# Optimization experiments

Hardware: AMD Instinct MI355X
Metric: run time of the kernel (lower is better)

Reference implementation:

```python
import jax, jax.numpy as jnp
import numpy as np

T, N, E, F, H, OUT = 6, 50000, 800000, 32, 64, 16


def _glorot(key, shape):
    lim = np.sqrt(6.0 / (shape[0] + shape[1])).astype(np.float32)
    return jax.random.uniform(key, shape, jnp.float32, -lim, lim)


def setup_inputs() -> dict:
    key = jax.random.key(0)
    ks = jax.random.split(key, 12)
    return {
        "xs": jax.random.normal(ks[0], (T, N, F), jnp.float32),
        "edge_index": jax.random.randint(ks[1], (T, 2, E), 0, N, jnp.int32),
        # GCNConv weights/biases for the z, r, h gates
        "Wz": _glorot(ks[2], (F, H)), "bz": jnp.zeros((H,), jnp.float32),
        "Wr": _glorot(ks[3], (F, H)), "br": jnp.zeros((H,), jnp.float32),
        "Wh": _glorot(ks[4], (F, H)), "bh": jnp.zeros((H,), jnp.float32),
        # Linear(2H -> H) per gate
        "Lz_W": _glorot(ks[5], (2 * H, H)), "Lz_b": jnp.zeros((H,), jnp.float32),
        "Lr_W": _glorot(ks[6], (2 * H, H)), "Lr_b": jnp.zeros((H,), jnp.float32),
        "Lh_W": _glorot(ks[7], (2 * H, H)), "Lh_b": jnp.zeros((H,), jnp.float32),
        # final Linear(H -> 16)
        "out_W": _glorot(ks[8], (H, OUT)), "out_b": jnp.zeros((OUT,), jnp.float32),
    }


def _gcn(x, W, b, src, dst):
    """GCNConv: D^-1/2 (A+I) D^-1/2 X W + b, edge list form."""
    n = x.shape[0]
    xw = x @ W  # [N,H] project first (cheaper than per-edge)
    loop = jnp.arange(n, dtype=src.dtype)
    s = jnp.concatenate([src, loop])
    d = jnp.concatenate([dst, loop])
    deg = jax.ops.segment_sum(jnp.ones_like(d, jnp.float32), d, num_segments=n)
    dinv = jnp.where(deg > 0, jax.lax.rsqrt(deg), 0.0)
    norm = dinv[s] * dinv[d]          # [E+N]
    msg = xw[s] * norm[:, None]       # gather + scale
    agg = jax.ops.segment_sum(msg, d, num_segments=n)  # scatter-add
    return agg + b


def reference(xs, edge_index, Wz, bz, Wr, br, Wh, bh,
              Lz_W, Lz_b, Lr_W, Lr_b, Lh_W, Lh_b, out_W, out_b):
    n = xs.shape[1]

    def step(h, inp):
        x, src, dst = inp
        Z = jax.nn.sigmoid(jnp.concatenate([_gcn(x, Wz, bz, src, dst), h], -1) @ Lz_W + Lz_b)
        R = jax.nn.sigmoid(jnp.concatenate([_gcn(x, Wr, br, src, dst), h], -1) @ Lr_W + Lr_b)
        Ht = jnp.tanh(jnp.concatenate([_gcn(x, Wh, bh, src, dst), h * R], -1) @ Lh_W + Lh_b)
        h_new = Z * h + (1.0 - Z) * Ht
        return h_new, None

    h0 = jnp.zeros((n, Wz.shape[1]), xs.dtype)
    h_final, _ = jax.lax.scan(step, h0, (xs, edge_index[:, 0], edge_index[:, 1]))
    return h_final @ out_W + out_b  # [N,16]
```

## Files before the change

kernel.cpp:

```cpp
#include <hip/hip_runtime.h>
#include <hip/hip_bf16.h>

#define TT 6
#define NN 50000
#define EE 800000
#define FF 32
#define HH 64
#define OO 16

#define NB 256
#define DPB 196
#define CHUNK 4096
#define CAP 4096

#define WFRAG_N 19456

typedef unsigned short ushort_t;
typedef unsigned char uchar_t;
typedef short short8 __attribute__((ext_vector_type(8)));
typedef float f32x4 __attribute__((ext_vector_type(4)));

__device__ __forceinline__ float ubf(ushort_t v){ return __uint_as_float(((unsigned)v) << 16); }
__device__ __forceinline__ ushort_t f2b(float f){
  unsigned u = __float_as_uint(f);
  return (ushort_t)((u + 0x7FFFu + ((u >> 16) & 1u)) >> 16);
}
__device__ __forceinline__ float lo16f(unsigned u){ return __uint_as_float(u << 16); }
__device__ __forceinline__ float hi16f(unsigned u){ return __uint_as_float(u & 0xFFFF0000u); }

__global__ void prepall_kernel(const float* __restrict__ Wz,const float* __restrict__ bz,
                               const float* __restrict__ Wr,const float* __restrict__ br,
                               const float* __restrict__ Wh,const float* __restrict__ bh,
                               const float* __restrict__ Lz,const float* __restrict__ Lzb,
                               const float* __restrict__ Lr,const float* __restrict__ Lrb,
                               const float* __restrict__ Lh,const float* __restrict__ Lhb,
                               const float* __restrict__ oW,const float* __restrict__ ob,
                               short* __restrict__ wfrag, float* __restrict__ wbias,
                               int* __restrict__ bcur){
  int bid = blockIdx.x, tid = threadIdx.x;
  if (bid < 76){
    int idx = bid*256 + tid;
    int slot = idx >> 9, lane = (idx >> 3) & 63, j = idx & 7;
    int q = lane >> 4, l15 = lane & 15;
    float val;
    if (slot < 36){
      int g, kc, ncol;
      if (slot < 24){ int nt = slot/3; kc = slot - nt*3; ncol = nt*16 + l15;
                      g = (ncol < 64) ? 0 : 1; ncol &= 63; }
      else          { int s2 = slot-24; int nt = s2/3; kc = s2 - nt*3;
                      ncol = nt*16 + l15; g = 2; }
      const float* W = (g==0)?Wz:((g==1)?Wr:Wh);
      const float* L = (g==0)?Lz:((g==1)?Lr:Lh);
      int k = kc*32 + q*8 + j;
      if (k < 32){
        float s = 0.f;
        for (int m = 0; m < 64; m++) s += W[k*64+m] * L[m*64+ncol];
        val = s;
      } else val = L[(32+k)*64 + ncol];
    } else {
      int kc = slot - 36;
      int k = kc*32 + q*8 + j;
      val = oW[k*16 + l15];
    }
    wfrag[idx] = (short)f2b(val);
  } else {
    if (tid < 192){
      int g = tid >> 6, j = tid & 63;
      const float* L  = (g==0)?Lz:((g==1)?Lr:Lh);
      const float* bb = (g==0)?bz:((g==1)?br:bh);
      const float* Lb = (g==0)?Lzb:((g==1)?Lrb:Lhb);
      float s = Lb[j];
      for (int m = 0; m < 64; m++) s += bb[m] * L[m*64+j];
      wbias[tid] = s;
    } else if (tid < 208){
      wbias[tid] = ob[tid-192];
    }
    for (int i = tid; i < 1536; i += 256) bcur[i] = 0;
  }
}

__global__ __launch_bounds__(256) void scatter_kernel(const int* __restrict__ ei,
                                                      int* __restrict__ bcur,
                                                      ushort_t* __restrict__ ssrc16,
                                                      uchar_t* __restrict__ sdst8){
  int t = blockIdx.y;
  __shared__ int cnt[NB];
  __shared__ int lstart[NB];
  __shared__ int gbase[NB];
  __shared__ int wsum[4];
  __shared__ ushort_t spay[CHUNK];
  __shared__ uchar_t  sdlo[CHUNK];
  __shared__ uchar_t  sbk[CHUNK];
  int tid = threadIdx.x;
  cnt[tid] = 0;
  __syncthreads();
  int e0 = blockIdx.x*CHUNK;
  const int* srcs = ei + t*2*EE;
  const int* dsts = ei + t*2*EE + EE;
  int pk[CHUNK/256];
  int ps[CHUNK/256];
  int pd[CHUNK/256];
  #pragma unroll
  for (int i = 0; i < CHUNK/256; i++){
    int e = e0 + i*256 + tid;
    if (e < EE){
      int s = srcs[e], d = dsts[e];
      int b = d / DPB;
      int lr = atomicAdd(&cnt[b], 1);
      pk[i] = (b << 12) | lr;
      ps[i] = s;
      pd[i] = d - b*DPB;
    } else pk[i] = -1;
  }
  __syncthreads();
  {
    int v = cnt[tid];
    int lane = tid & 63, wid = tid >> 6;
    int x = v;
    #pragma unroll
    for (int o = 1; o < 64; o <<= 1){
      int y = __shfl_up(x, o, 64);
      if (lane >= o) x += y;
    }
    if (lane == 63) wsum[wid] = x;
    __syncthreads();
    if (tid == 0){
      int s = 0;
      #pragma unroll
      for (int w = 0; w < 4; w++){ int tmp = wsum[w]; wsum[w] = s; s += tmp; }
    }
    __syncthreads();
    lstart[tid] = x - v + wsum[wid];
    gbase[tid] = (v > 0) ? atomicAdd(&bcur[t*NB + tid], v) : 0;
  }
  __syncthreads();
  #pragma unroll
  for (int i = 0; i < CHUNK/256; i++){
    if (pk[i] >= 0){
      int b = pk[i] >> 12, lr = pk[i] & 4095;
      int pos = lstart[b] + lr;
      spay[pos] = (ushort_t)ps[i];
      sdlo[pos] = (uchar_t)pd[i];
      sbk[pos]  = (uchar_t)b;
    }
  }
  __syncthreads();
  int nE = EE - e0; if (nE > CHUNK) nE = CHUNK;
  for (int i = tid; i < nE; i += 256){
    int b = sbk[i];
    int gpos = gbase[b] + (i - lstart[b]);
    if (gpos < CAP){
      size_t sb = (size_t)(t*NB + b)*CAP + gpos;
      ssrc16[sb] = spay[i];
      sdst8[sb]  = sdlo[i];
    }
  }
}

__global__ __launch_bounds__(256) void degdinv_kernel(const uchar_t* __restrict__ sdst8,
                                                      const int* __restrict__ bcur,
                                                      float* __restrict__ dinv){
  int b = blockIdx.x, t = blockIdx.y, tid = threadIdx.x;
  __shared__ int cnt[DPB];
  for (int i = tid; i < DPB; i += 256) cnt[i] = 0;
  __syncthreads();
  int ecnt = bcur[t*NB + b]; if (ecnt > CAP) ecnt = CAP;
  const uchar_t* dp = sdst8 + (size_t)(t*NB + b)*CAP;
  for (int i = tid; i < ecnt; i += 256)
    atomicAdd(&cnt[dp[i]], 1);
  __syncthreads();
  for (int i = tid; i < DPB; i += 256){
    int n = b*DPB + i;
    if (n < NN) dinv[t*NN + n] = rsqrtf((float)(cnt[i] + 1));
  }
}

__global__ void cvtscale_kernel(const float4* __restrict__ x4,
                                const float* __restrict__ dinv,
                                ushort4* __restrict__ xb4){
  int i = blockIdx.x*256 + threadIdx.x;
  if (i < TT*NN*8){
    float dn = dinv[i >> 3];
    float4 v = x4[i];
    ushort4 o;
    o.x = f2b(v.x*dn); o.y = f2b(v.y*dn); o.z = f2b(v.z*dn); o.w = f2b(v.w*dn);
    xb4[i] = o;
  }
}

__global__ __launch_bounds__(256) void gatherb_kernel(const ushort_t* __restrict__ xbs,
                                                      const ushort_t* __restrict__ ssrc16,
                                                      const uchar_t* __restrict__ sdst8,
                                                      const int* __restrict__ bcur,
                                                      ushort_t* __restrict__ aggb){
  int l = blockIdx.x;
  int wk = ((l & 7) * 192) + (l >> 3);
  int t = wk >> 8;
  int b = wk & 255;
  int tid = threadIdx.x;
  __shared__ ushort_t ssrc[CAP];
  __shared__ int scnt[DPB];
  __shared__ int soff[DPB + 1];
  __shared__ int scur[DPB];
  if (tid < DPB) scnt[tid] = 0;
  __syncthreads();
  int ecnt = bcur[t*NB + b]; if (ecnt > CAP) ecnt = CAP;
  size_t slab = (size_t)(t*NB + b)*CAP;
  const ushort_t* sp = ssrc16 + slab;
  const uchar_t*  dp = sdst8 + slab;
  for (int e = tid; e < ecnt; e += 256)
    atomicAdd(&scnt[dp[e]], 1);
  __syncthreads();
  if (tid < DPB) scur[tid] = scnt[tid];
  __syncthreads();
  for (int s = 1; s < DPB; s <<= 1){
    int v = 0;
    if (tid < DPB && tid >= s) v = scur[tid - s];
    __syncthreads();
    if (tid < DPB) scur[tid] += v;
    __syncthreads();
  }
  if (tid < DPB) soff[tid + 1] = scur[tid];
  if (tid == 0) soff[0] = 0;
  __syncthreads();
  if (tid < DPB) scur[tid] = soff[tid];
  __syncthreads();
  for (int e = tid; e < ecnt; e += 256){
    int ld = dp[e];
    int pos = atomicAdd(&scur[ld], 1);
    ssrc[pos] = sp[e];
  }
  __syncthreads();
  int wv = tid >> 6, lane = tid & 63;
  int g = lane >> 3, fp = lane & 7;
  const uint2* xb2 = (const uint2*)xbs + (size_t)t*NN*8;
  uint2* agg2 = (uint2*)aggb + (size_t)t*NN*8;
  for (int bb = wv; bb*8 < DPB; bb += 4){
    int ld = bb*8 + g;
    int e0 = 0, e1 = 0;
    if (ld < DPB){ e0 = soff[ld]; e1 = soff[ld + 1]; }
    float a0 = 0.f, a1 = 0.f, a2 = 0.f, a3 = 0.f;
    int i = e0;
    if (i < e1){
      int s = (int)ssrc[i];
      uint2 r = xb2[(size_t)s*8 + fp];
      for (++i; i < e1; ++i){
        int s2 = (int)ssrc[i];
        uint2 r2 = xb2[(size_t)s2*8 + fp];
        a0 += lo16f(r.x); a1 += hi16f(r.x);
        a2 += lo16f(r.y); a3 += hi16f(r.y);
        r = r2;
      }
      a0 += lo16f(r.x); a1 += hi16f(r.x);
      a2 += lo16f(r.y); a3 += hi16f(r.y);
    }
    int n = b*DPB + ld;
    if (ld < DPB && n < NN){
      float dn = rsqrtf((float)(e1 - e0 + 1));
      uint2 sv = xb2[(size_t)n*8 + fp];
      float o0 = dn*(a0 + lo16f(sv.x));
      float o1 = dn*(a1 + hi16f(sv.x));
      float o2 = dn*(a2 + lo16f(sv.y));
      float o3 = dn*(a3 + hi16f(sv.y));
      uint2 pk;
      pk.x = (unsigned)f2b(o0) | ((unsigned)f2b(o1) << 16);
      pk.y = (unsigned)f2b(o2) | ((unsigned)f2b(o3) << 16);
      agg2[(size_t)n*8 + fp] = pk;
    }
  }
}

__global__ __launch_bounds__(256) void gates_kernel(const ushort_t* __restrict__ aggb,
                                                    const float* __restrict__ wbias,
                                                    const short* __restrict__ wfrag,
                                                    float* __restrict__ out){
  __shared__ __align__(16) short As[2048];
  __shared__ __align__(16) short Hsp[4096];
  __shared__ __align__(16) short HRp[4096];
  int tid = threadIdx.x;
  int nb = blockIdx.x*64;
  int wv = tid >> 6, lane = tid & 63;
  int q = lane >> 4, l15 = lane & 15;
  #pragma unroll
  for (int r = 0; r < 8; r++) ((int*)Hsp)[tid + 256*r] = 0;
  short8 wz[3], wr[3], wh[3];
  #pragma unroll
  for (int kc = 0; kc < 3; kc++){
    wz[kc] = ((const short8*)wfrag)[(wv*3 + kc)*64 + lane];
    wr[kc] = ((const short8*)wfrag)[((wv+4)*3 + kc)*64 + lane];
    wh[kc] = ((const short8*)wfrag)[(24 + wv*3 + kc)*64 + lane];
  }
  int jz = wv*16 + l15;
  float cz = wbias[jz], cr = wbias[64 + jz], ch = wbias[128 + jz];
  int hidx = ((jz >> 3)*64)*8 + (jz & 7);
  f32x4 accZ[4], accR[4];
  for (int t = 0; t < TT; t++){
    {
      int n = tid >> 2, c = tid & 3, gn = nb + n;
      uint4 v = make_uint4(0,0,0,0);
      if (gn < NN) v = ((const uint4*)aggb)[((size_t)t*NN + gn)*4 + (size_t)c];
      *(uint4*)&As[(c*64 + n)*8] = v;
    }
    __syncthreads();
    #pragma unroll
    for (int mt = 0; mt < 4; mt++){
      short8 fa  = *(const short8*)&As [((q)*64   + mt*16 + l15)*8];
      short8 fh0 = *(const short8*)&Hsp[((q)*64   + mt*16 + l15)*8];
      short8 fh1 = *(const short8*)&Hsp[((4+q)*64 + mt*16 + l15)*8];
      f32x4 az = {0.f,0.f,0.f,0.f}, ar = {0.f,0.f,0.f,0.f};
      az = __builtin_amdgcn_mfma_f32_16x16x32_bf16(fa,  wz[0], az, 0,0,0);
      az = __builtin_amdgcn_mfma_f32_16x16x32_bf16(fh0, wz[1], az, 0,0,0);
      az = __builtin_amdgcn_mfma_f32_16x16x32_bf16(fh1, wz[2], az, 0,0,0);
      ar = __builtin_amdgcn_mfma_f32_16x16x32_bf16(fa,  wr[0], ar, 0,0,0);
      ar = __builtin_amdgcn_mfma_f32_16x16x32_bf16(fh0, wr[1], ar, 0,0,0);
      ar = __builtin_amdgcn_mfma_f32_16x16x32_bf16(fh1, wr[2], ar, 0,0,0);
      accZ[mt] = az; accR[mt] = ar;
    }
    #pragma unroll
    for (int mt = 0; mt < 4; mt++){
      #pragma unroll
      for (int e = 0; e < 4; e++){
        int node = mt*16 + q*4 + e;
        float z = 1.f/(1.f + __expf(-(accZ[mt][e] + cz)));
        float r = 1.f/(1.f + __expf(-(accR[mt][e] + cr)));
        float hold = ubf((ushort_t)Hsp[hidx + node*8]);
        HRp[hidx + node*8] = (short)f2b(hold * r);
        accZ[mt][e] = z;
      }
    }
    __syncthreads();
    #pragma unroll
    for (int mt = 0; mt < 4; mt++){
      short8 fa  = *(const short8*)&As [((q)*64   + mt*16 + l15)*8];
      short8 fr0 = *(const short8*)&HRp[((q)*64   + mt*16 + l15)*8];
      short8 fr1 = *(const short8*)&HRp[((4+q)*64 + mt*16 + l15)*8];
      f32x4 ahh = {0.f,0.f,0.f,0.f};
      ahh = __builtin_amdgcn_mfma_f32_16x16x32_bf16(fa,  wh[0], ahh, 0,0,0);
      ahh = __builtin_amdgcn_mfma_f32_16x16x32_bf16(fr0, wh[1], ahh, 0,0,0);
      ahh = __builtin_amdgcn_mfma_f32_16x16x32_bf16(fr1, wh[2], ahh, 0,0,0);
      accR[mt] = ahh;
    }
    float hn[4][4];
    #pragma unroll
    for (int mt = 0; mt < 4; mt++){
      #pragma unroll
      for (int e = 0; e < 4; e++){
        int node = mt*16 + q*4 + e;
        float xv = accR[mt][e] + ch;
        float ex = __expf(-2.f*fabsf(xv));
        float th = (1.f - ex)/(1.f + ex);
        th = (xv < 0.f) ? -th : th;
        float hold = ubf((ushort_t)Hsp[hidx + node*8]);
        float z = accZ[mt][e];
        hn[mt][e] = z*hold + (1.f - z)*th;
      }
    }
    __syncthreads();
    #pragma unroll
    for (int mt = 0; mt < 4; mt++){
      #pragma unroll
      for (int e = 0; e < 4; e++){
        int node = mt*16 + q*4 + e;
        Hsp[hidx + node*8] = (short)f2b(hn[mt][e]);
      }
    }
  }
  __syncthreads();
  short8 wo0 = ((const short8*)wfrag)[36*64 + lane];
  short8 wo1 = ((const short8*)wfrag)[37*64 + lane];
  short8 f0 = *(const short8*)&Hsp[((q)*64   + wv*16 + l15)*8];
  short8 f1 = *(const short8*)&Hsp[((4+q)*64 + wv*16 + l15)*8];
  f32x4 ao = {0.f,0.f,0.f,0.f};
  ao = __builtin_amdgcn_mfma_f32_16x16x32_bf16(f0, wo0, ao, 0,0,0);
  ao = __builtin_amdgcn_mfma_f32_16x16x32_bf16(f1, wo1, ao, 0,0,0);
  float ob = wbias[192 + l15];
  #pragma unroll
  for (int e = 0; e < 4; e++){
    int gn = nb + wv*16 + q*4 + e;
    if (gn < NN) out[gn*OO + l15] = ao[e] + ob;
  }
}

extern "C" void kernel_launch(void* const* d_in, const int* in_sizes, int n_in,
                              void* d_out, int out_size, void* d_ws, size_t ws_size,
                              hipStream_t stream) {
  const float* xs = (const float*)d_in[0];
  const int*   ei = (const int*)d_in[1];
  float* out = (float*)d_out;
  char* ws = (char*)d_ws;
  ushort_t*  aggb   = (ushort_t*)(ws + 0);
  ushort_t*  xbs    = (ushort_t*)(ws + 19200000);
  ushort_t*  ssrc16 = (ushort_t*)(ws + 38400000);
  uchar_t*   sdst8  = (uchar_t*) (ws + 50982912);
  float*     dinv   = (float*)   (ws + 57274368);
  int*       bcur   = (int*)     (ws + 58474368);
  short*     wfrag  = (short*)   (ws + 58480512);
  float*     wbias  = (float*)   (ws + 58519424);

  prepall_kernel<<<77, 256, 0, stream>>>(
      (const float*)d_in[2],(const float*)d_in[3],(const float*)d_in[4],(const float*)d_in[5],
      (const float*)d_in[6],(const float*)d_in[7],(const float*)d_in[8],(const float*)d_in[9],
      (const float*)d_in[10],(const float*)d_in[11],(const float*)d_in[12],(const float*)d_in[13],
      (const float*)d_in[14],(const float*)d_in[15], wfrag, wbias, bcur);
  scatter_kernel<<<dim3((EE + CHUNK-1)/CHUNK, TT), 256, 0, stream>>>(ei, bcur, ssrc16, sdst8);
  degdinv_kernel<<<dim3(NB, TT), 256, 0, stream>>>(sdst8, bcur, dinv);
  cvtscale_kernel<<<(TT*NN*8 + 255)/256, 256, 0, stream>>>((const float4*)xs, dinv, (ushort4*)xbs);
  gatherb_kernel<<<NB*TT, 256, 0, stream>>>(xbs, ssrc16, sdst8, bcur, aggb);
  gates_kernel<<<(NN + 63)/64, 256, 0, stream>>>(aggb, wbias, wfrag, out);
}
```

Baseline: 277.2 us.

## Keep hidden state in registers, load agg fragments directly, swizzle LDS layout

```diff
diff --git a/kernel.cpp b/kernel.cpp
--- a/kernel.cpp
+++ b/kernel.cpp
@@ -274,7 +274,6 @@
                                                     const float* __restrict__ wbias,
                                                     const short* __restrict__ wfrag,
                                                     float* __restrict__ out){
-  __shared__ __align__(16) short As[2048];
   __shared__ __align__(16) short Hsp[4096];
   __shared__ __align__(16) short HRp[4096];
   int tid = threadIdx.x;
@@ -292,84 +291,84 @@
   }
   int jz = wv*16 + l15;
   float cz = wbias[jz], cr = wbias[64 + jz], ch = wbias[128 + jz];
-  int hidx = ((jz >> 3)*64)*8 + (jz & 7);
-  f32x4 accZ[4], accR[4];
+  int c0 = jz >> 3, jl = jz & 7, x0 = c0 & 7;
+  int sq0 = q & 7, sq1 = (4 + q) & 7;
+  float hreg[4][4];
+  #pragma unroll
+  for (int mt = 0; mt < 4; mt++)
+    #pragma unroll
+    for (int e = 0; e < 4; e++) hreg[mt][e] = 0.f;
+  f32x4 accZ[4], accH[4];
+  const short8* agf = (const short8*)aggb;
   for (int t = 0; t < TT; t++){
-    {
-      int n = tid >> 2, c = tid & 3, gn = nb + n;
-      uint4 v = make_uint4(0,0,0,0);
-      if (gn < NN) v = ((const uint4*)aggb)[((size_t)t*NN + gn)*4 + (size_t)c];
-      *(uint4*)&As[(c*64 + n)*8] = v;
-    }
-    __syncthreads();
+    short8 fac[4];
     #pragma unroll
     for (int mt = 0; mt < 4; mt++){
-      short8 fa  = *(const short8*)&As [((q)*64   + mt*16 + l15)*8];
-      short8 fh0 = *(const short8*)&Hsp[((q)*64   + mt*16 + l15)*8];
-      short8 fh1 = *(const short8*)&Hsp[((4+q)*64 + mt*16 + l15)*8];
+      int gn = nb + mt*16 + l15;
+      short8 v = {0,0,0,0,0,0,0,0};
+      if (gn < NN) v = agf[((size_t)t*NN + gn)*4 + q];
+      fac[mt] = v;
+    }
+    __syncthreads();
+    #pragma unroll
+    for (int mt = 0; mt < 4; mt++){
+      int n = mt*16 + l15;
+      short8 fh0 = *(const short8*)&Hsp[((q)*64   + (n ^ sq0))*8];
+      short8 fh1 = *(const short8*)&Hsp[((4+q)*64 + (n ^ sq1))*8];
       f32x4 az = {0.f,0.f,0.f,0.f}, ar = {0.f,0.f,0.f,0.f};
-      az = __builtin_amdgcn_mfma_f32_16x16x32_bf16(fa,  wz[0], az, 0,0,0);
-      az = __builtin_amdgcn_mfma_f32_16x16x32_bf16(fh0, wz[1], az, 0,0,0);
-      az = __builtin_amdgcn_mfma_f32_16x16x32_bf16(fh1, wz[2], az, 0,0,0);
-      ar = __builtin_amdgcn_mfma_f32_16x16x32_bf16(fa,  wr[0], ar, 0,0,0);
-      ar = __builtin_amdgcn_mfma_f32_16x16x32_bf16(fh0, wr[1], ar, 0,0,0);
-      ar = __builtin_amdgcn_mfma_f32_16x16x32_bf16(fh1, wr[2], ar, 0,0,0);
-      accZ[mt] = az; accR[mt] = ar;
+      az = __builtin_amdgcn_mfma_f32_16x16x32_bf16(fac[mt], wz[0], az, 0,0,0);
+      az = __builtin_amdgcn_mfma_f32_16x16x32_bf16(fh0,     wz[1], az, 0,0,0);
+      az = __builtin_amdgcn_mfma_f32_16x16x32_bf16(fh1,     wz[2], az, 0,0,0);
+      ar = __builtin_amdgcn_mfma_f32_16x16x32_bf16(fac[mt], wr[0], ar, 0,0,0);
+      ar = __builtin_amdgcn_mfma_f32_16x16x32_bf16(fh0,     wr[1], ar, 0,0,0);
+      ar = __builtin_amdgcn_mfma_f32_16x16x32_bf16(fh1,     wr[2], ar, 0,0,0);
+      accZ[mt] = az; accH[mt] = ar;
     }
     #pragma unroll
     for (int mt = 0; mt < 4; mt++){
       #pragma unroll
       for (int e = 0; e < 4; e++){
         int node = mt*16 + q*4 + e;
-        float z = 1.f/(1.f + __expf(-(accZ[mt][e] + cz)));
-        float r = 1.f/(1.f + __expf(-(accR[mt][e] + cr)));
-        float hold = ubf((ushort_t)Hsp[hidx + node*8]);
-        HRp[hidx + node*8] = (short)f2b(hold * r);
+        float z = __builtin_amdgcn_rcpf(1.f + __expf(-(accZ[mt][e] + cz)));
+        float r = __builtin_amdgcn_rcpf(1.f + __expf(-(accH[mt][e] + cr)));
+        HRp[(c0*64 + (node ^ x0))*8 + jl] = (short)f2b(hreg[mt][e] * r);
         accZ[mt][e] = z;
       }
     }
     __syncthreads();
     #pragma unroll
     for (int mt = 0; mt < 4; mt++){
-      short8 fa  = *(const short8*)&As [((q)*64   + mt*16 + l15)*8];
-      short8 fr0 = *(const short8*)&HRp[((q)*64   + mt*16 + l15)*8];
-      short8 fr1 = *(const short8*)&HRp[((4+q)*64 + mt*16 + l15)*8];
+      int n = mt*16 + l15;
+      short8 fr0 = *(const short8*)&HRp[((q)*64   + (n ^ sq0))*8];
+      short8 fr1 = *(const short8*)&HRp[((4+q)*64 + (n ^ sq1))*8];
       f32x4 ahh = {0.f,0.f,0.f,0.f};
-      ahh = __builtin_amdgcn_mfma_f32_16x16x32_bf16(fa,  wh[0], ahh, 0,0,0);
-      ahh = __builtin_amdgcn_mfma_f32_16x16x32_bf16(fr0, wh[1], ahh, 0,0,0);
-      ahh = __builtin_amdgcn_mfma_f32_16x16x32_bf16(fr1, wh[2], ahh, 0,0,0);
-      accR[mt] = ahh;
-    }
-    float hn[4][4];
+      ahh = __builtin_amdgcn_mfma_f32_16x16x32_bf16(fac[mt], wh[0], ahh, 0,0,0);
+      ahh = __builtin_amdgcn_mfma_f32_16x16x32_bf16(fr0,     wh[1], ahh, 0,0,0);
+      ahh = __builtin_amdgcn_mfma_f32_16x16x32_bf16(fr1,     wh[2], ahh, 0,0,0);
+      accH[mt] = ahh;
+    }
     #pragma unroll
     for (int mt = 0; mt < 4; mt++){
       #pragma unroll
       for (int e = 0; e < 4; e++){
         int node = mt*16 + q*4 + e;
-        float xv = accR[mt][e] + ch;
+        float xv = accH[mt][e] + ch;
         float ex = __expf(-2.f*fabsf(xv));
-        float th = (1.f - ex)/(1.f + ex);
+        float th = (1.f - ex) * __builtin_amdgcn_rcpf(1.f + ex);
         th = (xv < 0.f) ? -th : th;
-        float hold = ubf((ushort_t)Hsp[hidx + node*8]);
         float z = accZ[mt][e];
-        hn[mt][e] = z*hold + (1.f - z)*th;
-      }
-    }
-    __syncthreads();
-    #pragma unroll
-    for (int mt = 0; mt < 4; mt++){
-      #pragma unroll
-      for (int e = 0; e < 4; e++){
-        int node = mt*16 + q*4 + e;
-        Hsp[hidx + node*8] = (short)f2b(hn[mt][e]);
+        float hv = z*hreg[mt][e] + (1.f - z)*th;
+        hreg[mt][e] = hv;
+        Hsp[(c0*64 + (node ^ x0))*8 + jl] = (short)f2b(hv);
       }
     }
   }
   __syncthreads();
   short8 wo0 = ((const short8*)wfrag)[36*64 + lane];
   short8 wo1 = ((const short8*)wfrag)[37*64 + lane];
-  short8 f0 = *(const short8*)&Hsp[((q)*64   + wv*16 + l15)*8];
-  short8 f1 = *(const short8*)&Hsp[((4+q)*64 + wv*16 + l15)*8];
+  int no = wv*16 + l15;
+  short8 f0 = *(const short8*)&Hsp[((q)*64   + (no ^ sq0))*8];
+  short8 f1 = *(const short8*)&Hsp[((4+q)*64 + (no ^ sq1))*8];
   f32x4 ao = {0.f,0.f,0.f,0.f};
   ao = __builtin_amdgcn_mfma_f32_16x16x32_bf16(f0, wo0, ao, 0,0,0);
   ao = __builtin_amdgcn_mfma_f32_16x16x32_bf16(f1, wo1, ao, 0,0,0);
```

Result: faster. 261.9 us (-5.5%).
